# Kernel tuning notes

Measured on AMD Instinct MI355X. Metric: run time of the kernel, lower is better.

Reference implementation:

```python
import jax, jax.numpy as jnp
import numpy as np


def quantize_uniform(x, n_bits, clip):
    # clamp to [-clip, clip], round to 2^(1-n_bits)*clip grid, cap at clip*(1-b)
    b = 2.0 ** (1 - n_bits)
    xc = jnp.clip(x, -clip, clip)
    return clip * jnp.minimum(b * jnp.round(xc / (b * clip)), 1.0 - b)


def quantize_act(x, n_bits, clip):
    # clip to [0, clip], round to 2^-n_bits grid, cap at 1 - 2^-n_bits
    s = 2.0 ** n_bits
    xc = jnp.clip(x, 0.0, clip)
    return jnp.minimum(jnp.round(xc * s) / s, 1.0 - 1.0 / s)


def qconv(x, w, b, pad):
    # fake-quantized conv: weights/bias quant(8,1), input quant(8,4), output quant(8,8)
    wq = quantize_uniform(w, 8, 1.0)
    bq = quantize_uniform(b, 8, 1.0)
    xq = quantize_uniform(x, 8, 4.0)
    y = jax.lax.conv_general_dilated(
        xq, wq, window_strides=(1, 1), padding=[(pad, pad), (pad, pad)],
        dimension_numbers=('NCHW', 'OIHW', 'NCHW'))
    y = y + bq[None, :, None, None]
    return quantize_uniform(y, 8, 8.0)


def setup_inputs() -> dict:
    key = jax.random.key(0)
    ks = jax.random.split(key, 7)
    N, Cin, H, W = 32, 128, 56, 56
    Sq, E1, E3 = 32, 128, 128
    x = jax.random.normal(ks[0], (N, Cin, H, W), dtype=jnp.float32)
    w_sq = jax.random.normal(ks[1], (Sq, Cin, 1, 1), dtype=jnp.float32) * 0.05
    b_sq = jax.random.normal(ks[2], (Sq,), dtype=jnp.float32) * 0.05
    w_e1 = jax.random.normal(ks[3], (E1, Sq, 1, 1), dtype=jnp.float32) * 0.05
    b_e1 = jax.random.normal(ks[4], (E1,), dtype=jnp.float32) * 0.05
    w_e3 = jax.random.normal(ks[5], (E3, Sq, 3, 3), dtype=jnp.float32) * 0.05
    b_e3 = jax.random.normal(ks[6], (E3,), dtype=jnp.float32) * 0.05
    return {'x': x, 'w_sq': w_sq, 'b_sq': b_sq, 'w_e1': w_e1, 'b_e1': b_e1,
            'w_e3': w_e3, 'b_e3': b_e3}


def reference(x, w_sq, b_sq, w_e1, b_e1, w_e3, b_e3):
    h = jax.nn.relu(qconv(x, w_sq, b_sq, pad=0))
    h = quantize_act(h, 13, 4.0)
    y1 = jax.nn.relu(qconv(h, w_e1, b_e1, pad=0))
    y3 = jax.nn.relu(qconv(h, w_e3, b_e3, pad=1))
    return jnp.concatenate([y1, y3], axis=1)
```

## Files before the change

kernel.cpp:

```cpp
#include <hip/hip_runtime.h>
#include <stdint.h>

typedef __bf16 bf16x8 __attribute__((ext_vector_type(8)));
typedef float  f32x4  __attribute__((ext_vector_type(4)));

#define HW   3136
#define WID  56
#define CIN  128
#define SQ   32
#define NPIX 100352

#define OFF_BSQ 0
#define OFF_BE  32
#define WSQF_BYTES_OFF 1152
#define WE1F_BYTES_OFF 9344
#define WE3F_BYTES_OFF 17536
#define HQ_BYTES_OFF   91264

__device__ __forceinline__ float quant_w8(float x){
  float xc = fminf(fmaxf(x,-1.f),1.f);
  return fminf(rintf(xc*128.f)*0.0078125f, 0.9921875f);
}
__device__ __forceinline__ ushort wq_int_bf16(float x){
  float xc = fminf(fmaxf(x,-1.f),1.f);
  float n = fminf(rintf(xc*128.f), 127.f);
  return (ushort)(__float_as_uint(n)>>16);
}
__device__ __forceinline__ uint pack2(uint k0, uint k1){
  return (__float_as_uint((float)k0)>>16) | (__float_as_uint((float)k1)&0xffff0000u);
}
__device__ __forceinline__ uint pack2f(float a, float b){
  return (__float_as_uint(a)>>16) | (__float_as_uint(b)&0xffff0000u);
}

__global__ void prep_kernel(const float* __restrict__ wsq, const float* __restrict__ bsq,
                            const float* __restrict__ we1, const float* __restrict__ be1,
                            const float* __restrict__ we3, const float* __restrict__ be3,
                            float* __restrict__ ws){
  int tid = blockIdx.x*blockDim.x+threadIdx.x;
  int nth = gridDim.x*blockDim.x;
  ushort* wsqf = (ushort*)((char*)ws + WSQF_BYTES_OFF);
  ushort* we1f = (ushort*)((char*)ws + WE1F_BYTES_OFF);
  ushort* we3f = (ushort*)((char*)ws + WE3F_BYTES_OFF);
  for (int i=tid;i<SQ;i+=nth) ws[OFF_BSQ+i]=quant_w8(bsq[i]);
  for (int i=tid;i<256;i+=nth) ws[OFF_BE+i] = (i<128)? quant_w8(be1[i]) : quant_w8(be3[i-128]);
  for (int i=tid;i<4096;i+=nth){
    int mfkc=i>>9, l=(i>>3)&63, j=i&7;
    int mf=mfkc>>2, kc=mfkc&3;
    int co=mf*16+(l&15), ci=kc*32+(l>>4)*8+j;
    wsqf[i] = wq_int_bf16(wsq[co*CIN+ci]);
  }
  for (int i=tid;i<4096;i+=nth){
    int mf=i>>9, l=(i>>3)&63, j=i&7;
    int co=mf*16+(l&15), ci=(l>>4)*8+j;
    we1f[i] = wq_int_bf16(we1[co*SQ+ci]);
  }
  for (int i=tid;i<36864;i+=nth){
    int mf=i/4608, r=i-mf*4608, t=r>>9, l=(r>>3)&63, j=r&7;
    int co=mf*16+(l&15), ci=(l>>4)*8+j;
    we3f[i] = wq_int_bf16(we3[(co*SQ+ci)*9+t]);
  }
}

__global__ __launch_bounds__(256) void squeeze_kernel(const float* __restrict__ x,
    const float* __restrict__ ws, uint8_t* __restrict__ hq){
  int tid = threadIdx.x, wid = tid>>6, lane = tid&63;
  int colg = lane&15, kg = lane>>4;

  int pixbase = (blockIdx.x*4 + wid)*16;
  int n = pixbase/HW;
  int rem = pixbase - n*HW + colg;
  const float* xp = x + (size_t)n*CIN*HW + rem;

  float xv[32];
  #pragma unroll
  for (int kc=0;kc<4;++kc)
    #pragma unroll
    for (int j=0;j<8;++j)
      xv[kc*8+j] = xp[(size_t)(kc*32 + kg*8 + j)*HW];

  const bf16x8* wsqf = (const bf16x8*)((const char*)ws + WSQF_BYTES_OFF);
  bf16x8 W[8];
  #pragma unroll
  for (int q=0;q<8;++q) W[q] = wsqf[q*64 + lane];

  bf16x8 Bf[4];
  #pragma unroll
  for (int kc=0;kc<4;++kc){
    float m[8];
    #pragma unroll
    for (int j=0;j<8;++j){
      float v = fminf(fmaxf(xv[kc*8+j],-4.f),4.f);
      m[j] = fminf(rintf(v*32.f), 127.f);
    }
    union { uint u[4]; bf16x8 v; } cv;
    #pragma unroll
    for (int q=0;q<4;++q) cv.u[q] = pack2f(m[q*2], m[q*2+1]);
    Bf[kc] = cv.v;
  }

  f32x4 acc0 = (f32x4){0.f,0.f,0.f,0.f};
  f32x4 acc1 = (f32x4){0.f,0.f,0.f,0.f};
  #pragma unroll
  for (int kc=0;kc<4;++kc){
    acc0 = __builtin_amdgcn_mfma_f32_16x16x32_bf16(W[kc],   Bf[kc], acc0, 0,0,0);
    acc1 = __builtin_amdgcn_mfma_f32_16x16x32_bf16(W[4+kc], Bf[kc], acc1, 0,0,0);
  }

  #pragma unroll
  for (int mf=0;mf<2;++mf){
    f32x4 a = mf ? acc1 : acc0;
    uint p=0;
    #pragma unroll
    for (int r=0;r<4;++r){
      float bias = ws[OFF_BSQ + mf*16 + kg*4 + r];
      float y = fmaf(a[r], 0.000244140625f, bias);
      y = fminf(fmaxf(y,-8.f),8.f);
      y = fminf(rintf(y*16.f)*0.0625f, 7.9375f);
      y = fmaxf(y,0.f);
      y = fminf(y,4.f);
      y = fminf(y,0.9998779296875f);
      uint mm = (uint)(int)rintf(y*32.f);
      p |= mm<<(8*r);
    }
    *(uint*)(hq + (size_t)(pixbase+colg)*32 + mf*16 + kg*4) = p;
  }
}

__global__ __launch_bounds__(256) void expand_kernel(const uint8_t* __restrict__ hq,
    const float* __restrict__ ws, float* __restrict__ out){
  __shared__ uint4 lds4[232*4];
  int br = blockIdx.x;
  int n  = blockIdx.y;
  int tid = threadIdx.x;

  if (tid < 232){
    int r = tid/58, c = tid - r*58;
    int gy = br*2 + r - 1, gx = c - 1;
    uint4 v0, v1;
    if ((unsigned)gy < 56u && (unsigned)gx < 56u){
      const uint4* src = (const uint4*)(hq + ((size_t)(n*HW + gy*WID + gx))*32);
      v0 = src[0]; v1 = src[1];
    } else { v0 = make_uint4(0,0,0,0); v1 = v0; }
    uint w8[8] = {v0.x,v0.y,v0.z,v0.w,v1.x,v1.y,v1.z,v1.w};
    #pragma unroll
    for (int cc=0;cc<4;++cc){
      uint a = w8[cc*2], b = w8[cc*2+1];
      uint4 o;
      o.x = pack2(a&255u, (a>>8)&255u);
      o.y = pack2((a>>16)&255u, a>>24);
      o.z = pack2(b&255u, (b>>8)&255u);
      o.w = pack2((b>>16)&255u, b>>24);
      lds4[tid*4 + (cc ^ ((tid>>1)&3))] = o;
    }
  }
  __syncthreads();

  int lane = tid&63, wid = tid>>6;
  int colg = lane&15, kg = lane>>4;
  int baseh[7];
  #pragma unroll
  for (int nf=0;nf<7;++nf){
    int p = nf*16 + colg;
    int row = p/56, xx = p - row*56;
    baseh[nf] = (row+1)*58 + xx + 1;
  }

  f32x4 acc[4][7];
  #pragma unroll
  for (int mi=0;mi<4;++mi)
    #pragma unroll
    for (int nf=0;nf<7;++nf)
      acc[mi][nf] = (f32x4){0.f,0.f,0.f,0.f};

  const bf16x8* we1f = (const bf16x8*)((const char*)ws + WE1F_BYTES_OFF);
  const bf16x8* we3f = (const bf16x8*)((const char*)ws + WE3F_BYTES_OFF);
  const bf16x8* lbase = (const bf16x8*)lds4;

  #pragma unroll
  for (int t=0;t<9;++t){
    int off = (t/3 - 1)*58 + (t%3 - 1);
    bf16x8 B[7];
    #pragma unroll
    for (int nf=0;nf<7;++nf){
      int ph = baseh[nf] + off;
      int idx = ph*4 + (kg ^ ((ph>>1)&3));
      B[nf] = lbase[idx];
    }
    bf16x8 A2 = we3f[(wid*9+t)*64 + lane];
    bf16x8 A3 = we3f[((wid+4)*9+t)*64 + lane];
    #pragma unroll
    for (int nf=0;nf<7;++nf){
      acc[2][nf] = __builtin_amdgcn_mfma_f32_16x16x32_bf16(B[nf], A2, acc[2][nf], 0,0,0);
      acc[3][nf] = __builtin_amdgcn_mfma_f32_16x16x32_bf16(B[nf], A3, acc[3][nf], 0,0,0);
    }
    if (t==4){
      bf16x8 A0 = we1f[wid*64 + lane];
      bf16x8 A1 = we1f[(wid+4)*64 + lane];
      #pragma unroll
      for (int nf=0;nf<7;++nf){
        acc[0][nf] = __builtin_amdgcn_mfma_f32_16x16x32_bf16(B[nf], A0, acc[0][nf], 0,0,0);
        acc[1][nf] = __builtin_amdgcn_mfma_f32_16x16x32_bf16(B[nf], A1, acc[1][nf], 0,0,0);
      }
    }
  }

  #pragma unroll
  for (int mi=0;mi<4;++mi){
    int co = (wid+mi*4)*16 + colg;
    float bias = ws[OFF_BE + co];
    float* opb = out + (size_t)(n*256+co)*HW + br*112 + kg*4;
    #pragma unroll
    for (int nf=0;nf<7;++nf){
      f32x4 a = acc[mi][nf];
      f32x4 yv;
      #pragma unroll
      for (int r=0;r<4;++r){
        float y = fmaf(a[r], 0.000244140625f, bias);
        y = fminf(fmaxf(y,-8.f),8.f);
        y = fminf(rintf(y*16.f)*0.0625f, 7.9375f);
        y = fmaxf(y,0.f);
        yv[r] = y;
      }
      *(f32x4*)(opb + nf*16) = yv;
    }
  }
}

extern "C" void kernel_launch(void* const* d_in, const int* in_sizes, int n_in,
                              void* d_out, int out_size, void* d_ws, size_t ws_size,
                              hipStream_t stream){
  const float* x   = (const float*)d_in[0];
  const float* wsq = (const float*)d_in[1];
  const float* bsq = (const float*)d_in[2];
  const float* we1 = (const float*)d_in[3];
  const float* be1 = (const float*)d_in[4];
  const float* we3 = (const float*)d_in[5];
  const float* be3 = (const float*)d_in[6];
  float* out = (float*)d_out;
  float* ws  = (float*)d_ws;
  uint8_t* hq = (uint8_t*)d_ws + HQ_BYTES_OFF;

  hipLaunchKernelGGL(prep_kernel, dim3(64), dim3(256), 0, stream,
                     wsq, bsq, we1, be1, we3, be3, ws);
  hipLaunchKernelGGL(squeeze_kernel, dim3(NPIX/64), dim3(256), 0, stream, x, ws, hq);
  hipLaunchKernelGGL(expand_kernel, dim3(28, 32), dim3(256), 0, stream, hq, ws, out);
}
```

Measured before the change: 47.45 us.

## Fuse squeeze and expand convs into one kernel with halo recompute in LDS

Merges the squeeze 1x1 conv and the expand 1x1/3x3 convs into one kernel. Each 512-thread block handles 8 output rows of one image: it computes the squeezed activations for those rows plus a one-row halo directly into LDS, then runs the expand MFMAs from LDS. This removes the global round trip of the intermediate tensor and one kernel launch. In exchange the halo rows are recomputed, the grid shrinks to 224 blocks, and register pressure per block rises.

```diff
diff --git a/kernel.cpp b/kernel.cpp
--- a/kernel.cpp
+++ b/kernel.cpp
@@ -8,14 +8,12 @@
 #define WID  56
 #define CIN  128
 #define SQ   32
-#define NPIX 100352
 
 #define OFF_BSQ 0
 #define OFF_BE  32
 #define WSQF_BYTES_OFF 1152
 #define WE1F_BYTES_OFF 9344
 #define WE3F_BYTES_OFF 17536
-#define HQ_BYTES_OFF   91264
 
 __device__ __forceinline__ float quant_w8(float x){
   float xc = fminf(fmaxf(x,-1.f),1.f);
@@ -25,9 +23,6 @@
   float xc = fminf(fmaxf(x,-1.f),1.f);
   float n = fminf(rintf(xc*128.f), 127.f);
   return (ushort)(__float_as_uint(n)>>16);
-}
-__device__ __forceinline__ uint pack2(uint k0, uint k1){
-  return (__float_as_uint((float)k0)>>16) | (__float_as_uint((float)k1)&0xffff0000u);
 }
 __device__ __forceinline__ uint pack2f(float a, float b){
   return (__float_as_uint(a)>>16) | (__float_as_uint(b)&0xffff0000u);
@@ -62,167 +57,167 @@
   }
 }
 
-__global__ __launch_bounds__(256) void squeeze_kernel(const float* __restrict__ x,
-    const float* __restrict__ ws, uint8_t* __restrict__ hq){
-  int tid = threadIdx.x, wid = tid>>6, lane = tid&63;
+__global__ __launch_bounds__(512, 2) void fire_kernel(const float* __restrict__ x,
+    const float* __restrict__ ws, float* __restrict__ out){
+  __shared__ uint4 lds4[2320];
+  int bry = blockIdx.x;
+  int n   = blockIdx.y;
+  int tid = threadIdx.x, w = tid>>6, lane = tid&63;
   int colg = lane&15, kg = lane>>4;
-
-  int pixbase = (blockIdx.x*4 + wid)*16;
-  int n = pixbase/HW;
-  int rem = pixbase - n*HW + colg;
-  const float* xp = x + (size_t)n*CIN*HW + rem;
-
-  float xv[32];
-  #pragma unroll
-  for (int kc=0;kc<4;++kc)
-    #pragma unroll
-    for (int j=0;j<8;++j)
-      xv[kc*8+j] = xp[(size_t)(kc*32 + kg*8 + j)*HW];
-
-  const bf16x8* wsqf = (const bf16x8*)((const char*)ws + WSQF_BYTES_OFF);
-  bf16x8 W[8];
-  #pragma unroll
-  for (int q=0;q<8;++q) W[q] = wsqf[q*64 + lane];
-
-  bf16x8 Bf[4];
-  #pragma unroll
-  for (int kc=0;kc<4;++kc){
-    float m[8];
-    #pragma unroll
-    for (int j=0;j<8;++j){
-      float v = fminf(fmaxf(xv[kc*8+j],-4.f),4.f);
-      m[j] = fminf(rintf(v*32.f), 127.f);
-    }
-    union { uint u[4]; bf16x8 v; } cv;
-    #pragma unroll
-    for (int q=0;q<4;++q) cv.u[q] = pack2f(m[q*2], m[q*2+1]);
-    Bf[kc] = cv.v;
-  }
-
-  f32x4 acc0 = (f32x4){0.f,0.f,0.f,0.f};
-  f32x4 acc1 = (f32x4){0.f,0.f,0.f,0.f};
-  #pragma unroll
-  for (int kc=0;kc<4;++kc){
-    acc0 = __builtin_amdgcn_mfma_f32_16x16x32_bf16(W[kc],   Bf[kc], acc0, 0,0,0);
-    acc1 = __builtin_amdgcn_mfma_f32_16x16x32_bf16(W[4+kc], Bf[kc], acc1, 0,0,0);
-  }
-
-  #pragma unroll
-  for (int mf=0;mf<2;++mf){
-    f32x4 a = mf ? acc1 : acc0;
-    uint p=0;
-    #pragma unroll
-    for (int r=0;r<4;++r){
-      float bias = ws[OFF_BSQ + mf*16 + kg*4 + r];
-      float y = fmaf(a[r], 0.000244140625f, bias);
-      y = fminf(fmaxf(y,-8.f),8.f);
-      y = fminf(rintf(y*16.f)*0.0625f, 7.9375f);
-      y = fmaxf(y,0.f);
-      y = fminf(y,4.f);
-      y = fminf(y,0.9998779296875f);
-      uint mm = (uint)(int)rintf(y*32.f);
-      p |= mm<<(8*r);
-    }
-    *(uint*)(hq + (size_t)(pixbase+colg)*32 + mf*16 + kg*4) = p;
-  }
-}
-
-__global__ __launch_bounds__(256) void expand_kernel(const uint8_t* __restrict__ hq,
-    const float* __restrict__ ws, float* __restrict__ out){
-  __shared__ uint4 lds4[232*4];
-  int br = blockIdx.x;
-  int n  = blockIdx.y;
-  int tid = threadIdx.x;
-
-  if (tid < 232){
-    int r = tid/58, c = tid - r*58;
-    int gy = br*2 + r - 1, gx = c - 1;
-    uint4 v0, v1;
-    if ((unsigned)gy < 56u && (unsigned)gx < 56u){
-      const uint4* src = (const uint4*)(hq + ((size_t)(n*HW + gy*WID + gx))*32);
-      v0 = src[0]; v1 = src[1];
-    } else { v0 = make_uint4(0,0,0,0); v1 = v0; }
-    uint w8[8] = {v0.x,v0.y,v0.z,v0.w,v1.x,v1.y,v1.z,v1.w};
-    #pragma unroll
-    for (int cc=0;cc<4;++cc){
-      uint a = w8[cc*2], b = w8[cc*2+1];
-      uint4 o;
-      o.x = pack2(a&255u, (a>>8)&255u);
-      o.y = pack2((a>>16)&255u, a>>24);
-      o.z = pack2(b&255u, (b>>8)&255u);
-      o.w = pack2((b>>16)&255u, b>>24);
-      lds4[tid*4 + (cc ^ ((tid>>1)&3))] = o;
-    }
-  }
+  int R0 = bry*8;
+  int vr0 = (R0==0) ? 0 : R0-1;
+  int vr1 = (R0+8 > 55) ? 55 : R0+8;
+  int limit = (vr1+1)*WID;
+  int nblk = ((vr1-vr0+1)*WID + 15)>>4;
+  int base_px = vr0*WID;
+
+  uint4 z = make_uint4(0,0,0,0);
+  for (int i=tid; i<2320; i+=512) lds4[i] = z;
   __syncthreads();
 
-  int lane = tid&63, wid = tid>>6;
-  int colg = lane&15, kg = lane>>4;
-  int baseh[7];
-  #pragma unroll
-  for (int nf=0;nf<7;++nf){
-    int p = nf*16 + colg;
-    int row = p/56, xx = p - row*56;
-    baseh[nf] = (row+1)*58 + xx + 1;
-  }
-
-  f32x4 acc[4][7];
-  #pragma unroll
-  for (int mi=0;mi<4;++mi)
-    #pragma unroll
-    for (int nf=0;nf<7;++nf)
-      acc[mi][nf] = (f32x4){0.f,0.f,0.f,0.f};
-
+  {
+    const bf16x8* wsqf = (const bf16x8*)((const char*)ws + WSQF_BYTES_OFF);
+    bf16x8 W[8];
+    #pragma unroll
+    for (int q=0;q<8;++q) W[q] = wsqf[q*64 + lane];
+    float bias[2][4];
+    #pragma unroll
+    for (int mf=0;mf<2;++mf)
+      #pragma unroll
+      for (int r=0;r<4;++r) bias[mf][r] = ws[OFF_BSQ + mf*16 + kg*4 + r];
+
+    for (int b=w; b<nblk; b+=8){
+      int px = base_px + b*16 + colg;
+      int pxc = (px < limit) ? px : (limit-1);
+      const float* xp = x + (size_t)n*CIN*HW + pxc;
+      float xv[32];
+      #pragma unroll
+      for (int kc=0;kc<4;++kc)
+        #pragma unroll
+        for (int j=0;j<8;++j)
+          xv[kc*8+j] = xp[(size_t)(kc*32 + kg*8 + j)*HW];
+
+      bf16x8 Bf[4];
+      #pragma unroll
+      for (int kc=0;kc<4;++kc){
+        float m[8];
+        #pragma unroll
+        for (int j=0;j<8;++j){
+          float v = fminf(fmaxf(xv[kc*8+j],-4.f),4.f);
+          m[j] = fminf(rintf(v*32.f), 127.f);
+        }
+        union { uint u[4]; bf16x8 v; } cv;
+        #pragma unroll
+        for (int q=0;q<4;++q) cv.u[q] = pack2f(m[q*2], m[q*2+1]);
+        Bf[kc] = cv.v;
+      }
+
+      f32x4 acc0 = (f32x4){0.f,0.f,0.f,0.f};
+      f32x4 acc1 = (f32x4){0.f,0.f,0.f,0.f};
+      #pragma unroll
+      for (int kc=0;kc<4;++kc){
+        acc0 = __builtin_amdgcn_mfma_f32_16x16x32_bf16(W[kc],   Bf[kc], acc0, 0,0,0);
+        acc1 = __builtin_amdgcn_mfma_f32_16x16x32_bf16(W[4+kc], Bf[kc], acc1, 0,0,0);
+      }
+
+      if (px < limit){
+        int rr = px/WID, c = px - rr*WID;
+        int ph = (rr - R0 + 1)*58 + c + 1;
+        #pragma unroll
+        for (int mf=0;mf<2;++mf){
+          f32x4 a = mf ? acc1 : acc0;
+          float m[4];
+          #pragma unroll
+          for (int r=0;r<4;++r){
+            float y = fmaf(a[r], 0.000244140625f, bias[mf][r]);
+            y = fminf(fmaxf(y,-8.f),8.f);
+            y = fminf(rintf(y*16.f)*0.0625f, 7.9375f);
+            y = fmaxf(y,0.f);
+            y = fminf(y,4.f);
+            y = fminf(y,0.9998779296875f);
+            m[r] = rintf(y*32.f);
+          }
+          int chunk = mf*2 + (kg>>1);
+          int idx = ph*4 + (chunk ^ ((ph>>1)&3));
+          uint* dst = (uint*)&lds4[idx] + (kg&1)*2;
+          dst[0] = pack2f(m[0], m[1]);
+          dst[1] = pack2f(m[2], m[3]);
+        }
+      }
+    }
+  }
+  __syncthreads();
+
+  int wid = w&3, rpl = w>>2;
   const bf16x8* we1f = (const bf16x8*)((const char*)ws + WE1F_BYTES_OFF);
   const bf16x8* we3f = (const bf16x8*)((const char*)ws + WE3F_BYTES_OFF);
   const bf16x8* lbase = (const bf16x8*)lds4;
 
   #pragma unroll
-  for (int t=0;t<9;++t){
-    int off = (t/3 - 1)*58 + (t%3 - 1);
-    bf16x8 B[7];
+  for (int s=0; s<2; ++s){
+    int rp = rpl*2 + s;
+    int baseh[7];
     #pragma unroll
     for (int nf=0;nf<7;++nf){
-      int ph = baseh[nf] + off;
-      int idx = ph*4 + (kg ^ ((ph>>1)&3));
-      B[nf] = lbase[idx];
-    }
-    bf16x8 A2 = we3f[(wid*9+t)*64 + lane];
-    bf16x8 A3 = we3f[((wid+4)*9+t)*64 + lane];
-    #pragma unroll
-    for (int nf=0;nf<7;++nf){
-      acc[2][nf] = __builtin_amdgcn_mfma_f32_16x16x32_bf16(B[nf], A2, acc[2][nf], 0,0,0);
-      acc[3][nf] = __builtin_amdgcn_mfma_f32_16x16x32_bf16(B[nf], A3, acc[3][nf], 0,0,0);
-    }
-    if (t==4){
-      bf16x8 A0 = we1f[wid*64 + lane];
-      bf16x8 A1 = we1f[(wid+4)*64 + lane];
+      int p = rp*112 + nf*16 + colg;
+      int rr = p/WID, c = p - rr*WID;
+      baseh[nf] = (rr+1)*58 + c + 1;
+    }
+
+    f32x4 acc[4][7];
+    #pragma unroll
+    for (int mi=0;mi<4;++mi)
+      #pragma unroll
+      for (int nf=0;nf<7;++nf)
+        acc[mi][nf] = (f32x4){0.f,0.f,0.f,0.f};
+
+    #pragma unroll
+    for (int t=0;t<9;++t){
+      int off = (t/3 - 1)*58 + (t%3 - 1);
+      bf16x8 B[7];
       #pragma unroll
       for (int nf=0;nf<7;++nf){
-        acc[0][nf] = __builtin_amdgcn_mfma_f32_16x16x32_bf16(B[nf], A0, acc[0][nf], 0,0,0);
-        acc[1][nf] = __builtin_amdgcn_mfma_f32_16x16x32_bf16(B[nf], A1, acc[1][nf], 0,0,0);
-      }
-    }
-  }
-
-  #pragma unroll
-  for (int mi=0;mi<4;++mi){
-    int co = (wid+mi*4)*16 + colg;
-    float bias = ws[OFF_BE + co];
-    float* opb = out + (size_t)(n*256+co)*HW + br*112 + kg*4;
-    #pragma unroll
-    for (int nf=0;nf<7;++nf){
-      f32x4 a = acc[mi][nf];
-      f32x4 yv;
-      #pragma unroll
-      for (int r=0;r<4;++r){
-        float y = fmaf(a[r], 0.000244140625f, bias);
-        y = fminf(fmaxf(y,-8.f),8.f);
-        y = fminf(rintf(y*16.f)*0.0625f, 7.9375f);
-        y = fmaxf(y,0.f);
-        yv[r] = y;
-      }
-      *(f32x4*)(opb + nf*16) = yv;
+        int ph = baseh[nf] + off;
+        int idx = ph*4 + (kg ^ ((ph>>1)&3));
+        B[nf] = lbase[idx];
+      }
+      bf16x8 A2 = we3f[(wid*9+t)*64 + lane];
+      bf16x8 A3 = we3f[((wid+4)*9+t)*64 + lane];
+      #pragma unroll
+      for (int nf=0;nf<7;++nf){
+        acc[2][nf] = __builtin_amdgcn_mfma_f32_16x16x32_bf16(B[nf], A2, acc[2][nf], 0,0,0);
+        acc[3][nf] = __builtin_amdgcn_mfma_f32_16x16x32_bf16(B[nf], A3, acc[3][nf], 0,0,0);
+      }
+      if (t==4){
+        bf16x8 A0 = we1f[wid*64 + lane];
+        bf16x8 A1 = we1f[(wid+4)*64 + lane];
+        #pragma unroll
+        for (int nf=0;nf<7;++nf){
+          acc[0][nf] = __builtin_amdgcn_mfma_f32_16x16x32_bf16(B[nf], A0, acc[0][nf], 0,0,0);
+          acc[1][nf] = __builtin_amdgcn_mfma_f32_16x16x32_bf16(B[nf], A1, acc[1][nf], 0,0,0);
+        }
+      }
+    }
+
+    #pragma unroll
+    for (int mi=0;mi<4;++mi){
+      int co = (wid+mi*4)*16 + colg;
+      float bias = ws[OFF_BE + co];
+      float* opb = out + (size_t)(n*256+co)*HW + R0*WID + rp*112 + kg*4;
+      #pragma unroll
+      for (int nf=0;nf<7;++nf){
+        f32x4 a = acc[mi][nf];
+        f32x4 yv;
+        #pragma unroll
+        for (int r=0;r<4;++r){
+          float y = fmaf(a[r], 0.000244140625f, bias);
+          y = fminf(fmaxf(y,-8.f),8.f);
+          y = fminf(rintf(y*16.f)*0.0625f, 7.9375f);
+          y = fmaxf(y,0.f);
+          yv[r] = y;
+        }
+        *(f32x4*)(opb + nf*16) = yv;
+      }
     }
   }
 }
@@ -239,10 +234,8 @@
   const float* be3 = (const float*)d_in[6];
   float* out = (float*)d_out;
   float* ws  = (float*)d_ws;
-  uint8_t* hq = (uint8_t*)d_ws + HQ_BYTES_OFF;
 
   hipLaunchKernelGGL(prep_kernel, dim3(64), dim3(256), 0, stream,
                      wsq, bsq, we1, be1, we3, be3, ws);
-  hipLaunchKernelGGL(squeeze_kernel, dim3(NPIX/64), dim3(256), 0, stream, x, ws, hq);
-  hipLaunchKernelGGL(expand_kernel, dim3(28, 32), dim3(256), 0, stream, hq, ws, out);
-}
+  hipLaunchKernelGGL(fire_kernel, dim3(7, 32), dim3(512), 0, stream, x, ws, out);
+}
```

New measurement: 43.40 us. 8.5% less time.

## Store squeeze output as padded bf16 and read expand operands from global

Applied to the files above, without the earlier changes.

The squeeze kernel now writes its intermediate activations as bf16 into a zero-padded 58x58 spatial layout, replacing the packed uint8 format. The expand kernel drops its LDS staging, byte-to-bf16 conversion and barrier, and loads MFMA B operands straight from global memory, relying on the padding to avoid boundary checks. The cost is a memset of the padded buffer on every call, twice the intermediate bytes, and nine times the global/L2 reads per tap instead of one shared-memory staging pass.

```diff
diff --git a/kernel.cpp b/kernel.cpp
--- a/kernel.cpp
+++ b/kernel.cpp
@@ -9,6 +9,7 @@
 #define CIN  128
 #define SQ   32
 #define NPIX 100352
+#define PHW  3364
 
 #define OFF_BSQ 0
 #define OFF_BE  32
@@ -25,9 +26,6 @@
   float xc = fminf(fmaxf(x,-1.f),1.f);
   float n = fminf(rintf(xc*128.f), 127.f);
   return (ushort)(__float_as_uint(n)>>16);
-}
-__device__ __forceinline__ uint pack2(uint k0, uint k1){
-  return (__float_as_uint((float)k0)>>16) | (__float_as_uint((float)k1)&0xffff0000u);
 }
 __device__ __forceinline__ uint pack2f(float a, float b){
   return (__float_as_uint(a)>>16) | (__float_as_uint(b)&0xffff0000u);
@@ -63,7 +61,7 @@
 }
 
 __global__ __launch_bounds__(256) void squeeze_kernel(const float* __restrict__ x,
-    const float* __restrict__ ws, uint8_t* __restrict__ hq){
+    const float* __restrict__ ws, ushort* __restrict__ hq){
   int tid = threadIdx.x, wid = tid>>6, lane = tid&63;
   int colg = lane&15, kg = lane>>4;
 
@@ -107,63 +105,43 @@
     acc1 = __builtin_amdgcn_mfma_f32_16x16x32_bf16(W[4+kc], Bf[kc], acc1, 0,0,0);
   }
 
+  int row = rem/WID, col = rem - row*WID;
+  size_t phq = (size_t)n*PHW + (row+1)*58 + (col+1);
   #pragma unroll
   for (int mf=0;mf<2;++mf){
     f32x4 a = mf ? acc1 : acc0;
-    uint p=0;
+    float bias[4], m[4];
     #pragma unroll
     for (int r=0;r<4;++r){
-      float bias = ws[OFF_BSQ + mf*16 + kg*4 + r];
-      float y = fmaf(a[r], 0.000244140625f, bias);
+      bias[r] = ws[OFF_BSQ + mf*16 + kg*4 + r];
+      float y = fmaf(a[r], 0.000244140625f, bias[r]);
       y = fminf(fmaxf(y,-8.f),8.f);
       y = fminf(rintf(y*16.f)*0.0625f, 7.9375f);
       y = fmaxf(y,0.f);
       y = fminf(y,4.f);
       y = fminf(y,0.9998779296875f);
-      uint mm = (uint)(int)rintf(y*32.f);
-      p |= mm<<(8*r);
-    }
-    *(uint*)(hq + (size_t)(pixbase+colg)*32 + mf*16 + kg*4) = p;
-  }
-}
-
-__global__ __launch_bounds__(256) void expand_kernel(const uint8_t* __restrict__ hq,
+      m[r] = rintf(y*32.f);
+    }
+    uint2 p;
+    p.x = pack2f(m[0], m[1]);
+    p.y = pack2f(m[2], m[3]);
+    *(uint2*)(hq + phq*32 + mf*16 + kg*4) = p;
+  }
+}
+
+__global__ __launch_bounds__(256) void expand_kernel(const ushort* __restrict__ hq,
     const float* __restrict__ ws, float* __restrict__ out){
-  __shared__ uint4 lds4[232*4];
-  int br = blockIdx.x;
-  int n  = blockIdx.y;
-  int tid = threadIdx.x;
-
-  if (tid < 232){
-    int r = tid/58, c = tid - r*58;
-    int gy = br*2 + r - 1, gx = c - 1;
-    uint4 v0, v1;
-    if ((unsigned)gy < 56u && (unsigned)gx < 56u){
-      const uint4* src = (const uint4*)(hq + ((size_t)(n*HW + gy*WID + gx))*32);
-      v0 = src[0]; v1 = src[1];
-    } else { v0 = make_uint4(0,0,0,0); v1 = v0; }
-    uint w8[8] = {v0.x,v0.y,v0.z,v0.w,v1.x,v1.y,v1.z,v1.w};
-    #pragma unroll
-    for (int cc=0;cc<4;++cc){
-      uint a = w8[cc*2], b = w8[cc*2+1];
-      uint4 o;
-      o.x = pack2(a&255u, (a>>8)&255u);
-      o.y = pack2((a>>16)&255u, a>>24);
-      o.z = pack2(b&255u, (b>>8)&255u);
-      o.w = pack2((b>>16)&255u, b>>24);
-      lds4[tid*4 + (cc ^ ((tid>>1)&3))] = o;
-    }
-  }
-  __syncthreads();
-
-  int lane = tid&63, wid = tid>>6;
+  int bry = blockIdx.x;
+  int n   = blockIdx.y;
+  int tid = threadIdx.x, wid = tid>>6, lane = tid&63;
   int colg = lane&15, kg = lane>>4;
+
   int baseh[7];
   #pragma unroll
   for (int nf=0;nf<7;++nf){
-    int p = nf*16 + colg;
-    int row = p/56, xx = p - row*56;
-    baseh[nf] = (row+1)*58 + xx + 1;
+    int p = bry*112 + nf*16 + colg;
+    int rr = p/WID, c = p - rr*WID;
+    baseh[nf] = (rr+1)*58 + c + 1;
   }
 
   f32x4 acc[4][7];
@@ -175,18 +153,15 @@
 
   const bf16x8* we1f = (const bf16x8*)((const char*)ws + WE1F_BYTES_OFF);
   const bf16x8* we3f = (const bf16x8*)((const char*)ws + WE3F_BYTES_OFF);
-  const bf16x8* lbase = (const bf16x8*)lds4;
+  const bf16x8* hb = (const bf16x8*)hq + (size_t)n*PHW*4 + kg;
 
   #pragma unroll
   for (int t=0;t<9;++t){
     int off = (t/3 - 1)*58 + (t%3 - 1);
     bf16x8 B[7];
     #pragma unroll
-    for (int nf=0;nf<7;++nf){
-      int ph = baseh[nf] + off;
-      int idx = ph*4 + (kg ^ ((ph>>1)&3));
-      B[nf] = lbase[idx];
-    }
+    for (int nf=0;nf<7;++nf)
+      B[nf] = hb[(size_t)(baseh[nf] + off)*4];
     bf16x8 A2 = we3f[(wid*9+t)*64 + lane];
     bf16x8 A3 = we3f[((wid+4)*9+t)*64 + lane];
     #pragma unroll
@@ -209,7 +184,7 @@
   for (int mi=0;mi<4;++mi){
     int co = (wid+mi*4)*16 + colg;
     float bias = ws[OFF_BE + co];
-    float* opb = out + (size_t)(n*256+co)*HW + br*112 + kg*4;
+    float* opb = out + (size_t)(n*256+co)*HW + bry*112 + kg*4;
     #pragma unroll
     for (int nf=0;nf<7;++nf){
       f32x4 a = acc[mi][nf];
@@ -239,10 +214,11 @@
   const float* be3 = (const float*)d_in[6];
   float* out = (float*)d_out;
   float* ws  = (float*)d_ws;
-  uint8_t* hq = (uint8_t*)d_ws + HQ_BYTES_OFF;
+  ushort* hq = (ushort*)((char*)d_ws + HQ_BYTES_OFF);
 
   hipLaunchKernelGGL(prep_kernel, dim3(64), dim3(256), 0, stream,
                      wsq, bsq, we1, be1, we3, be3, ws);
+  hipMemsetAsync(hq, 0, (size_t)32*PHW*64, stream);
   hipLaunchKernelGGL(squeeze_kernel, dim3(NPIX/64), dim3(256), 0, stream, x, ws, hq);
   hipLaunchKernelGGL(expand_kernel, dim3(28, 32), dim3(256), 0, stream, hq, ws, out);
 }
```

Result: slower. 59.92 us (+26.3%).
